# Performance work log

Measured on AMD Instinct MI355X. Metric: run time of the kernel, lower is better.

## Reference

```python
import jax, jax.numpy as jnp
import numpy as np

T, B, H = 2048, 32, 1024
L1, L2, L3 = 100, 10, 1  # cascade 100 -> 10 -> 1 from linear_size=100


def setup_inputs() -> dict:
    key = jax.random.key(0)
    ks = jax.random.split(key, 8)
    def lin_init(k, fan_in, shape):
        # torch nn.Linear default: U(-1/sqrt(fan_in), 1/sqrt(fan_in))
        bound = 1.0 / np.sqrt(fan_in)
        return jax.random.uniform(k, shape, jnp.float32, -bound, bound)
    return {
        "encoder_output": jax.random.normal(ks[0], (T, B, H), jnp.float32),
        "lengths": jax.random.randint(ks[1], (B,), 1, T + 1, jnp.int64),
        "W1": lin_init(ks[2], H, (L1, H)),
        "b1": lin_init(ks[3], H, (L1,)),
        "W2": lin_init(ks[4], L1, (L2, L1)),
        "b2": lin_init(ks[5], L1, (L2,)),
        "W3": lin_init(ks[6], L2, (L3, L2)),
        "b3": lin_init(ks[7], L2, (L3,)),
    }


def reference(encoder_output, lengths, W1, b1, W2, b2, W3, b3):
    # MLP cascade over all timesteps/batch at once: [T,B,H] -> [T,B,1]
    h = jax.nn.relu(jnp.einsum("tbh,lh->tbl", encoder_output, W1) + b1)
    h = jax.nn.relu(jnp.einsum("tbl,ml->tbm", h, W2) + b2)
    logits = jnp.einsum("tbm,om->tbo", h, W3) + b3  # [T,B,1]
    logp = jax.nn.log_sigmoid(logits)[..., 0]       # [T,B]
    # Mask timesteps beyond each sample's length, sum, exponentiate
    mask = jnp.arange(T)[:, None] < lengths[None, :]  # [T,B]
    return jnp.exp(jnp.sum(jnp.where(mask, logp, 0.0), axis=0))  # [B]
```

## Files before the change

kernel.cpp:

```cpp
#include <hip/hip_runtime.h>
#include <stdint.h>


#define T_DIM 2048
#define B_DIM 32
#define H_DIM 1024
#define L1_DIM 100
#define L1_PAD 112
#define L2_DIM 10
#define L2_PAD 16
#define K2_PAD 128
#define NBLK  512
#define TSLOT 512

#define W1B_ELEMS (L1_PAD * H_DIM)
#define W2B_ELEMS (L2_PAD * K2_PAD)
#define PART_OFF_BYTES ((W1B_ELEMS + W2B_ELEMS) * 2)

typedef float v4f __attribute__((ext_vector_type(4)));
typedef short s8  __attribute__((ext_vector_type(8)));

static __device__ __forceinline__ unsigned short f2bf(float f) {
    unsigned int u = __float_as_uint(f);
    u += 0x7fffu + ((u >> 16) & 1u);
    return (unsigned short)(u >> 16);
}

__global__ void convert_weights(const float* __restrict__ W1,
                                const float* __restrict__ W2,
                                unsigned short* __restrict__ wsb) {
    int i = blockIdx.x * 256 + threadIdx.x;
    if (i < W1B_ELEMS) {
        int row = i >> 10, col = i & 1023;
        float v = (row < L1_DIM) ? W1[row * H_DIM + col] : 0.0f;
        wsb[i] = f2bf(v);
    } else {
        int j = i - W1B_ELEMS;
        if (j < W2B_ELEMS) {
            int r = j >> 7, c = j & 127;
            float v = (r < L2_DIM && c < L1_DIM) ? W2[r * L1_DIM + c] : 0.0f;
            wsb[W1B_ELEMS + j] = f2bf(v);
        }
    }
}

__global__ __launch_bounds__(512, 4) void mlp_main(
    const float* __restrict__ enc,
    const int*   __restrict__ lenp,
    const float* __restrict__ b1,
    const float* __restrict__ b2,
    const float* __restrict__ W3,
    const float* __restrict__ b3,
    const unsigned short* __restrict__ w1b,
    const unsigned short* __restrict__ w2b,
    float* __restrict__ partials)
{
    __shared__ __align__(16) unsigned short bufB[2][L1_PAD * 64];
    __shared__ __align__(16) unsigned short ldsH[128 * 128];
    __shared__ float ldsPart[4][32];

    const int tid  = threadIdx.x;
    const int blk  = blockIdx.x;
    const int lane = tid & 63;
    const int w    = tid >> 6;
    const int m    = lane & 15;
    const int q    = lane >> 4;
    const int mx   = m & 7;

    const bool is64 = (lenp[1] == 0);

    const int slot = w >> 1;
    const int tA   = blk + TSLOT * slot;
    const int bA   = ((w & 1) << 4) + m;
    const int lenA = is64 ? lenp[2 * bA] : lenp[bA];
    const bool predA   = (tA < lenA);
    const bool waveAct = (__ballot(predA) != 0ull);

    float b1v[7];
#pragma unroll
    for (int nt = 0; nt < 7; ++nt) {
        int n = nt * 16 + m;
        b1v[nt] = (n < L1_DIM) ? b1[n] : 0.0f;
    }
    const float b2v = (m < L2_DIM) ? b2[m] : 0.0f;
    const float w3v = (m < L2_DIM) ? W3[m] : 0.0f;
    const float b3s = b3[0];

    const float* aptr = enc + (size_t)(tA * B_DIM + bA) * H_DIM + (q << 3);

    {
        int r  = (w << 4) + (lane >> 2);
        int c  = 14 + ((lane >> 1) & 1);
        int cl = c ^ (r & 7);
        *(uint2*)&ldsH[(r << 7) + (cl << 3) + ((lane & 1) << 2)] = make_uint2(0u, 0u);
    }

    auto stageW1 = [&](int buf, int kc) {
#pragma unroll
        for (int rep = 0; rep < 2; ++rep) {
            const int s = w + (rep << 3);
            if (s < 14) {
                const int idx = (s << 6) + lane;
                const int r   = idx >> 3;
                const int cg  = (idx & 7) ^ (r & 7);
                const unsigned short* gsrc =
                    w1b + (r << 10) + (kc << 6) + (cg << 3);
                __builtin_amdgcn_global_load_lds(
                    (const __attribute__((address_space(1))) unsigned int*)gsrc,
                    (__attribute__((address_space(3))) unsigned int*)&bufB[buf][s << 9],
                    16, 0, 0);
            }
        }
    };

    float4 xc0, xc1, xc2, xc3, xn0, xn1, xn2, xn3;
    auto loadX = [&](int kc, float4& a, float4& b, float4& c, float4& d) {
        if (predA) {
            const float* p = aptr + (kc << 6);
            a = *(const float4*)(p);
            b = *(const float4*)(p + 4);
            c = *(const float4*)(p + 32);
            d = *(const float4*)(p + 36);
        } else {
            a = b = c = d = make_float4(0.f, 0.f, 0.f, 0.f);
        }
    };

    v4f acc[7];
#pragma unroll
    for (int nt = 0; nt < 7; ++nt) acc[nt] = (v4f)0.0f;

    stageW1(0, 0);
    loadX(0, xc0, xc1, xc2, xc3);
    xn0 = xn1 = xn2 = xn3 = make_float4(0.f, 0.f, 0.f, 0.f);

    const int v0   = ((q ^ mx) << 3);
    const int v1   = (((4 + q) ^ mx) << 3);
    const int mrow = m << 6;

#pragma unroll
    for (int kc = 0; kc < 16; ++kc) {
        const int cur = kc & 1;
        __syncthreads();
        if (kc < 15) {
            stageW1(cur ^ 1, kc + 1);
            loadX(kc + 1, xn0, xn1, xn2, xn3);
        }
        if (waveAct) {
            const unsigned short* bb = &bufB[cur][mrow];
#pragma unroll
            for (int ks = 0; ks < 2; ++ks) {
                const float4 lo = ks ? xc2 : xc0;
                const float4 hi = ks ? xc3 : xc1;
                s8 af;
                af[0] = (short)f2bf(lo.x); af[1] = (short)f2bf(lo.y);
                af[2] = (short)f2bf(lo.z); af[3] = (short)f2bf(lo.w);
                af[4] = (short)f2bf(hi.x); af[5] = (short)f2bf(hi.y);
                af[6] = (short)f2bf(hi.z); af[7] = (short)f2bf(hi.w);
                const int vo = ks ? v1 : v0;
#pragma unroll
                for (int nt = 0; nt < 7; ++nt) {
                    const s8 bf = *(const s8*)(bb + (nt << 10) + vo);
                    acc[nt] = __builtin_amdgcn_mfma_f32_16x16x32_bf16(
                        af, bf, acc[nt], 0, 0, 0);
                }
            }
        }
        xc0 = xn0; xc1 = xn1; xc2 = xn2; xc3 = xn3;
    }

#pragma unroll
    for (int nt = 0; nt < 7; ++nt) {
#pragma unroll
        for (int reg = 0; reg < 4; ++reg) {
            const float h  = fmaxf(acc[nt][reg] + b1v[nt], 0.0f);
            const int row  = (w << 4) + (q << 2) + reg;
            const int col  = (nt << 4) + m;
            const int cl   = (col >> 3) ^ (row & 7);
            ldsH[(row << 7) + (cl << 3) + (col & 7)] = f2bf(h);
        }
    }

    v4f acc2 = (v4f)0.0f;
    {
        const unsigned short* hb = &ldsH[((w << 4) + m) << 7];
#pragma unroll
        for (int ks = 0; ks < 4; ++ks) {
            const int cl = ((ks << 2) + q) ^ mx;
            const s8 a2  = *(const s8*)(hb + (cl << 3));
            const s8 b2f = *(const s8*)(w2b + (m << 7) + (ks << 5) + (q << 3));
            acc2 = __builtin_amdgcn_mfma_f32_16x16x32_bf16(a2, b2f, acc2, 0, 0, 0);
        }
    }

    v4f z;
#pragma unroll
    for (int reg = 0; reg < 4; ++reg) {
        const float y2 = fmaxf(acc2[reg] + b2v, 0.0f);
        z[reg] = y2 * w3v;
    }
#pragma unroll
    for (int msk = 1; msk < 16; msk <<= 1) {
#pragma unroll
        for (int reg = 0; reg < 4; ++reg)
            z[reg] += __shfl_xor(z[reg], msk, 16);
    }
    if (m == 0) {
#pragma unroll
        for (int reg = 0; reg < 4; ++reg) {
            const int rowLocal = (q << 2) + reg;
            const int bC   = ((w & 1) << 4) + rowLocal;
            const int lenC = is64 ? lenp[2 * bC] : lenp[bC];
            const float logit = z[reg] + b3s;
            const float logp  = fminf(logit, 0.0f) - log1pf(__expf(-fabsf(logit)));
            ldsPart[slot][bC] = (tA < lenC) ? logp : 0.0f;
        }
    }
    __syncthreads();
    if (tid < 32)
        partials[tid * NBLK + blk] =
            ldsPart[0][tid] + ldsPart[1][tid] + ldsPart[2][tid] + ldsPart[3][tid];
}

__global__ void finalize(const float* __restrict__ partials,
                         float* __restrict__ out) {
    const int b = blockIdx.x;
    const int tid = threadIdx.x;
    float s = 0.0f;
    for (int i = tid; i < NBLK; i += 256) s += partials[b * NBLK + i];
#pragma unroll
    for (int off = 32; off > 0; off >>= 1) s += __shfl_down(s, off, 64);
    __shared__ float red[4];
    if ((tid & 63) == 0) red[tid >> 6] = s;
    __syncthreads();
    if (tid == 0) out[b] = expf(red[0] + red[1] + red[2] + red[3]);
}

extern "C" void kernel_launch(void* const* d_in, const int* in_sizes, int n_in,
                              void* d_out, int out_size, void* d_ws, size_t ws_size,
                              hipStream_t stream) {
    const float* enc = (const float*)d_in[0];
    const int*   len = (const int*)d_in[1];
    const float* W1  = (const float*)d_in[2];
    const float* b1  = (const float*)d_in[3];
    const float* W2  = (const float*)d_in[4];
    const float* b2  = (const float*)d_in[5];
    const float* W3  = (const float*)d_in[6];
    const float* b3  = (const float*)d_in[7];

    unsigned short* wsb = (unsigned short*)d_ws;
    float* partials = (float*)((char*)d_ws + PART_OFF_BYTES);
    float* out = (float*)d_out;

    convert_weights<<<(W1B_ELEMS + W2B_ELEMS + 255) / 256, 256, 0, stream>>>(W1, W2, wsb);
    mlp_main<<<NBLK, 512, 0, stream>>>(enc, len, b1, b2, W3, b3,
                                       wsb, wsb + W1B_ELEMS, partials);
    finalize<<<B_DIM, 256, 0, stream>>>(partials, out);
}
```

Baseline: 361.6 us.

## Remap waves to batch-major timestep tiles to skip masked work past lengths

Reassigns each wave to a single batch element and 16 consecutive timesteps so that tiles entirely beyond a sample's length skip loads and MFMA work, with whole blocks exiting early. Per-wave partial sums are written directly, removing the shared-memory reduction, and finalize shrinks to one wave per batch. This trades some intra-block load balance for skipping the masked half of the encoder reads.

```diff
diff --git a/kernel.cpp b/kernel.cpp
--- a/kernel.cpp
+++ b/kernel.cpp
@@ -11,7 +11,7 @@
 #define L2_PAD 16
 #define K2_PAD 128
 #define NBLK  512
-#define TSLOT 512
+#define NTG   128
 
 #define W1B_ELEMS (L1_PAD * H_DIM)
 #define W2B_ELEMS (L2_PAD * K2_PAD)
@@ -57,7 +57,6 @@
 {
     __shared__ __align__(16) unsigned short bufB[2][L1_PAD * 64];
     __shared__ __align__(16) unsigned short ldsH[128 * 128];
-    __shared__ float ldsPart[4][32];
 
     const int tid  = threadIdx.x;
     const int blk  = blockIdx.x;
@@ -69,12 +68,17 @@
 
     const bool is64 = (lenp[1] == 0);
 
-    const int slot = w >> 1;
-    const int tA   = blk + TSLOT * slot;
-    const int bA   = ((w & 1) << 4) + m;
-    const int lenA = is64 ? lenp[2 * bA] : lenp[bA];
-    const bool predA   = (tA < lenA);
-    const bool waveAct = (__ballot(predA) != 0ull);
+    const int b    = (w << 2) + (blk >> 7);
+    const int tg   = (blk + (w << 4)) & 127;
+    const int t0   = tg << 4;
+    const int lenW = is64 ? lenp[2 * b] : lenp[b];
+    const bool waveAct = (t0 < lenW);
+    const bool predA   = (t0 + m < lenW);
+
+    if (__syncthreads_count((int)waveAct) == 0) {
+        if (lane == 0) partials[(b << 7) + tg] = 0.0f;
+        return;
+    }
 
     float b1v[7];
 #pragma unroll
@@ -86,7 +90,7 @@
     const float w3v = (m < L2_DIM) ? W3[m] : 0.0f;
     const float b3s = b3[0];
 
-    const float* aptr = enc + (size_t)(tA * B_DIM + bA) * H_DIM + (q << 3);
+    const float* aptr = enc + ((size_t)(t0 + m) * B_DIM + b) * H_DIM + (q << 3);
 
     {
         int r  = (w << 4) + (lane >> 2);
@@ -114,15 +118,15 @@
     };
 
     float4 xc0, xc1, xc2, xc3, xn0, xn1, xn2, xn3;
-    auto loadX = [&](int kc, float4& a, float4& b, float4& c, float4& d) {
+    auto loadX = [&](int kc, float4& a, float4& bb_, float4& c, float4& d) {
         if (predA) {
             const float* p = aptr + (kc << 6);
-            a = *(const float4*)(p);
-            b = *(const float4*)(p + 4);
-            c = *(const float4*)(p + 32);
-            d = *(const float4*)(p + 36);
+            a   = *(const float4*)(p);
+            bb_ = *(const float4*)(p + 4);
+            c   = *(const float4*)(p + 32);
+            d   = *(const float4*)(p + 36);
         } else {
-            a = b = c = d = make_float4(0.f, 0.f, 0.f, 0.f);
+            a = bb_ = c = d = make_float4(0.f, 0.f, 0.f, 0.f);
         }
     };
 
@@ -169,71 +173,68 @@
         xc0 = xn0; xc1 = xn1; xc2 = xn2; xc3 = xn3;
     }
 
-#pragma unroll
-    for (int nt = 0; nt < 7; ++nt) {
+    float s = 0.0f;
+    if (waveAct) {
+#pragma unroll
+        for (int nt = 0; nt < 7; ++nt) {
+#pragma unroll
+            for (int reg = 0; reg < 4; ++reg) {
+                const float h  = fmaxf(acc[nt][reg] + b1v[nt], 0.0f);
+                const int row  = (w << 4) + (q << 2) + reg;
+                const int col  = (nt << 4) + m;
+                const int cl   = (col >> 3) ^ (row & 7);
+                ldsH[(row << 7) + (cl << 3) + (col & 7)] = f2bf(h);
+            }
+        }
+
+        v4f acc2 = (v4f)0.0f;
+        {
+            const unsigned short* hb = &ldsH[((w << 4) + m) << 7];
+#pragma unroll
+            for (int ks = 0; ks < 4; ++ks) {
+                const int cl = ((ks << 2) + q) ^ mx;
+                const s8 a2  = *(const s8*)(hb + (cl << 3));
+                const s8 b2f = *(const s8*)(w2b + (m << 7) + (ks << 5) + (q << 3));
+                acc2 = __builtin_amdgcn_mfma_f32_16x16x32_bf16(a2, b2f, acc2, 0, 0, 0);
+            }
+        }
+
+        v4f z;
 #pragma unroll
         for (int reg = 0; reg < 4; ++reg) {
-            const float h  = fmaxf(acc[nt][reg] + b1v[nt], 0.0f);
-            const int row  = (w << 4) + (q << 2) + reg;
-            const int col  = (nt << 4) + m;
-            const int cl   = (col >> 3) ^ (row & 7);
-            ldsH[(row << 7) + (cl << 3) + (col & 7)] = f2bf(h);
-        }
-    }
-
-    v4f acc2 = (v4f)0.0f;
-    {
-        const unsigned short* hb = &ldsH[((w << 4) + m) << 7];
-#pragma unroll
-        for (int ks = 0; ks < 4; ++ks) {
-            const int cl = ((ks << 2) + q) ^ mx;
-            const s8 a2  = *(const s8*)(hb + (cl << 3));
-            const s8 b2f = *(const s8*)(w2b + (m << 7) + (ks << 5) + (q << 3));
-            acc2 = __builtin_amdgcn_mfma_f32_16x16x32_bf16(a2, b2f, acc2, 0, 0, 0);
-        }
-    }
-
-    v4f z;
-#pragma unroll
-    for (int reg = 0; reg < 4; ++reg) {
-        const float y2 = fmaxf(acc2[reg] + b2v, 0.0f);
-        z[reg] = y2 * w3v;
-    }
-#pragma unroll
-    for (int msk = 1; msk < 16; msk <<= 1) {
-#pragma unroll
-        for (int reg = 0; reg < 4; ++reg)
-            z[reg] += __shfl_xor(z[reg], msk, 16);
-    }
-    if (m == 0) {
+            const float y2 = fmaxf(acc2[reg] + b2v, 0.0f);
+            z[reg] = y2 * w3v;
+        }
+#pragma unroll
+        for (int msk = 1; msk < 16; msk <<= 1) {
+#pragma unroll
+            for (int reg = 0; reg < 4; ++reg)
+                z[reg] += __shfl_xor(z[reg], msk, 16);
+        }
+        float part = 0.0f;
 #pragma unroll
         for (int reg = 0; reg < 4; ++reg) {
             const int rowLocal = (q << 2) + reg;
-            const int bC   = ((w & 1) << 4) + rowLocal;
-            const int lenC = is64 ? lenp[2 * bC] : lenp[bC];
-            const float logit = z[reg] + b3s;
-            const float logp  = fminf(logit, 0.0f) - log1pf(__expf(-fabsf(logit)));
-            ldsPart[slot][bC] = (tA < lenC) ? logp : 0.0f;
-        }
-    }
-    __syncthreads();
-    if (tid < 32)
-        partials[tid * NBLK + blk] =
-            ldsPart[0][tid] + ldsPart[1][tid] + ldsPart[2][tid] + ldsPart[3][tid];
+            if (t0 + rowLocal < lenW) {
+                const float logit = z[reg] + b3s;
+                part += fminf(logit, 0.0f) - log1pf(__expf(-fabsf(logit)));
+            }
+        }
+        part += __shfl_xor(part, 16);
+        part += __shfl_xor(part, 32);
+        s = part;
+    }
+    if (lane == 0) partials[(b << 7) + tg] = s;
 }
 
 __global__ void finalize(const float* __restrict__ partials,
                          float* __restrict__ out) {
     const int b = blockIdx.x;
-    const int tid = threadIdx.x;
-    float s = 0.0f;
-    for (int i = tid; i < NBLK; i += 256) s += partials[b * NBLK + i];
+    const int lane = threadIdx.x;
+    float s = partials[(b << 7) + lane] + partials[(b << 7) + 64 + lane];
 #pragma unroll
     for (int off = 32; off > 0; off >>= 1) s += __shfl_down(s, off, 64);
-    __shared__ float red[4];
-    if ((tid & 63) == 0) red[tid >> 6] = s;
-    __syncthreads();
-    if (tid == 0) out[b] = expf(red[0] + red[1] + red[2] + red[3]);
+    if (lane == 0) out[b] = expf(s);
 }
 
 extern "C" void kernel_launch(void* const* d_in, const int* in_sizes, int n_in,
@@ -255,5 +256,5 @@
     convert_weights<<<(W1B_ELEMS + W2B_ELEMS + 255) / 256, 256, 0, stream>>>(W1, W2, wsb);
     mlp_main<<<NBLK, 512, 0, stream>>>(enc, len, b1, b2, W3, b3,
                                        wsb, wsb + W1B_ELEMS, partials);
-    finalize<<<B_DIM, 256, 0, stream>>>(partials, out);
-}
+    finalize<<<B_DIM, 64, 0, stream>>>(partials, out);
+}
```

New measurement: 362.4 us. About the same (+0.2%).
